# Kernel optimization log

Measured on AMD Instinct MI355X. Metric: run time of the kernel, lower is better.

The kernel has to match this reference:

```python
import jax, jax.numpy as jnp
import numpy as np

D = 768
H = 8
HD = D // H  # 96
DFF = 2048
EPS = 1e-5


def layernorm(x, g, b):
    mu = jnp.mean(x, axis=-1, keepdims=True)
    var = jnp.var(x, axis=-1, keepdims=True)
    return (x - mu) * jax.lax.rsqrt(var + EPS) * g + b


def setup_inputs() -> dict:
    key = jax.random.key(0)
    ks = jax.random.split(key, 12)
    B, L = 4, 1024
    s = lambda fan: 1.0 / np.sqrt(fan)
    return {
        "x": jax.random.normal(ks[0], (B, L, D), jnp.float32),
        "attn_bias": jax.random.normal(ks[1], (B, L, L), jnp.float32),
        "in_proj_w": jax.random.normal(ks[2], (3 * D, D), jnp.float32) * s(D),
        "in_proj_b": jnp.zeros((3 * D,), jnp.float32),
        "out_w": jax.random.normal(ks[3], (D, D), jnp.float32) * s(D),
        "out_b": jnp.zeros((D,), jnp.float32),
        "ff1_w": jax.random.normal(ks[4], (DFF, D), jnp.float32) * s(D),
        "ff1_b": jnp.zeros((DFF,), jnp.float32),
        "ff2_w": jax.random.normal(ks[5], (D, DFF), jnp.float32) * s(DFF),
        "ff2_b": jnp.zeros((D,), jnp.float32),
        "ln1_g": jnp.ones((D,), jnp.float32),
        "ln1_b": jnp.zeros((D,), jnp.float32),
        "ln2_g": jnp.ones((D,), jnp.float32),
        "ln2_b": jnp.zeros((D,), jnp.float32),
    }


def reference(x, attn_bias, in_proj_w, in_proj_b, out_w, out_b,
              ff1_w, ff1_b, ff2_w, ff2_b, ln1_g, ln1_b, ln2_g, ln2_b):
    B, L, _ = x.shape
    # combined QKV projection (torch nn.MultiheadAttention in_proj)
    qkv = x @ in_proj_w.T + in_proj_b  # [B,L,3D]
    q, k, v = jnp.split(qkv, 3, axis=-1)
    q = q.reshape(B, L, H, HD).transpose(0, 2, 1, 3)  # [B,H,L,hd]
    k = k.reshape(B, L, H, HD).transpose(0, 2, 1, 3)
    v = v.reshape(B, L, H, HD).transpose(0, 2, 1, 3)
    scale = 1.0 / np.sqrt(HD)
    scores = jnp.einsum('bhld,bhmd->bhlm', q, k) * scale + attn_bias[:, None, :, :]
    probs = jax.nn.softmax(scores, axis=-1)
    attn = jnp.einsum('bhlm,bhmd->bhld', probs, v)  # [B,H,L,hd]
    attn = attn.transpose(0, 2, 1, 3).reshape(B, L, D)
    attn = attn @ out_w.T + out_b
    x = layernorm(x + attn, ln1_g, ln1_b)
    h = jax.nn.gelu(x @ ff1_w.T + ff1_b, approximate=False) @ ff2_w.T + ff2_b
    x = layernorm(x + h, ln2_g, ln2_b)
    return x
```

## Files before the change

### kernel.cpp

```cpp
#include <hip/hip_runtime.h>

typedef __bf16 bf16x8 __attribute__((ext_vector_type(8)));
typedef float f32x4 __attribute__((ext_vector_type(4)));
typedef unsigned short u16x8 __attribute__((ext_vector_type(8)));
typedef short s16x4 __attribute__((ext_vector_type(4)));

__device__ __forceinline__ unsigned short f2b(float f) {
    union { float f; unsigned u; } v; v.f = f;
    unsigned r = (v.u + 0x7fffu + ((v.u >> 16) & 1u)) >> 16;
    return (unsigned short)r;
}

__device__ __forceinline__ void load_lds16(const void* g, void* l) {
    __builtin_amdgcn_global_load_lds(
        (const __attribute__((address_space(1))) unsigned int*)g,
        (__attribute__((address_space(3))) unsigned int*)l,
        16, 0, 0);
}

__global__ void cvt5_kernel(const float* __restrict__ s0, const float* __restrict__ s1,
                            const float* __restrict__ s2, const float* __restrict__ s3,
                            const float* __restrict__ s4,
                            unsigned short* __restrict__ d0, unsigned short* __restrict__ d1,
                            unsigned short* __restrict__ d2, unsigned short* __restrict__ d3,
                            unsigned short* __restrict__ d4) {
    int i = blockIdx.x * 256 + threadIdx.x;
    const float* s; unsigned short* d; int off;
    if (i < 786432)       { s = s0; d = d0; off = 0; }
    else if (i < 1228800) { s = s1; d = d1; off = 786432; }
    else if (i < 1376256) { s = s2; d = d2; off = 1228800; }
    else if (i < 1769472) { s = s3; d = d3; off = 1376256; }
    else                  { s = s4; d = d4; off = 1769472; }
    i -= off;
    f32x4 v = ((const f32x4*)s)[i];
    s16x4 o;
    o.x = (short)f2b(v.x);
    o.y = (short)f2b(v.y);
    o.z = (short)f2b(v.z);
    o.w = (short)f2b(v.w);
    ((s16x4*)d)[i] = o;
}

template <int EPI>
__global__ __launch_bounds__(256, 5)
void gemm_ho(const unsigned short* __restrict__ A, const unsigned short* __restrict__ Bm,
             const float* __restrict__ bias, void* __restrict__ Cout,
             int M, int N, int K) {
    __shared__ unsigned short As[2][64 * 64];
    __shared__ unsigned short Bs[2][64 * 64];
    const int tid = threadIdx.x, lane = tid & 63, wid = tid >> 6;
    const int l15 = lane & 15, lq = lane >> 4;
    const int wr = wid >> 1, wc = wid & 1;

    const int nwg = gridDim.x * gridDim.y;
    int bid = blockIdx.y * gridDim.x + blockIdx.x;
    bid = (bid & 7) * (nwg >> 3) + (bid >> 3);
    const int bx = bid % gridDim.x, by = bid / gridDim.x;
    const int m0 = by * 64, n0 = bx * 64;

    const int srow = lane >> 3;
    const int scol = ((lane & 7) ^ srow) * 8;
    const int sw = (l15 & 7) << 4;

    f32x4 acc[2][2];
#pragma unroll
    for (int i = 0; i < 2; i++)
#pragma unroll
        for (int j = 0; j < 2; j++) acc[i][j] = 0.0f;

    auto stage = [&](int buf, int kt) {
        const int kb = kt * 64;
#pragma unroll
        for (int i = 0; i < 4; ++i) {
            const int c = wid * 4 + i;
            if (c < 8) {
                load_lds16(A + (size_t)(m0 + c * 8 + srow) * K + kb + scol,
                           (char*)As[buf] + c * 1024);
            } else {
                load_lds16(Bm + (size_t)(n0 + (c - 8) * 8 + srow) * K + kb + scol,
                           (char*)Bs[buf] + (c - 8) * 1024);
            }
        }
    };

    auto compute = [&](int buf) {
#pragma unroll
        for (int kc = 0; kc < 2; ++kc) {
            const int cb = kc * 64;
            bf16x8 af[2], bf[2];
#pragma unroll
            for (int mi = 0; mi < 2; mi++) {
                const int row = wr * 32 + mi * 16 + l15;
                af[mi] = *(const bf16x8*)((const char*)As[buf] + row * 128 + ((cb + lq * 16) ^ sw));
            }
#pragma unroll
            for (int ni = 0; ni < 2; ni++) {
                const int row = wc * 32 + ni * 16 + l15;
                bf[ni] = *(const bf16x8*)((const char*)Bs[buf] + row * 128 + ((cb + lq * 16) ^ sw));
            }
#pragma unroll
            for (int mi = 0; mi < 2; mi++)
#pragma unroll
                for (int ni = 0; ni < 2; ni++)
                    acc[mi][ni] = __builtin_amdgcn_mfma_f32_16x16x32_bf16(af[mi], bf[ni], acc[mi][ni], 0, 0, 0);
        }
    };

    const int nkt = K / 64;
    stage(0, 0);
    stage(1, 1);
    asm volatile("s_waitcnt vmcnt(4)" ::: "memory");
    __builtin_amdgcn_s_barrier();
    int cur = 0;
    for (int t = 0; t < nkt; ++t) {
        compute(cur);
        __builtin_amdgcn_s_barrier();
        if (t + 2 < nkt) {
            stage(cur, t + 2);
            asm volatile("s_waitcnt vmcnt(4)" ::: "memory");
        } else if (t + 1 < nkt) {
            asm volatile("s_waitcnt vmcnt(0)" ::: "memory");
        }
        if (t + 1 < nkt) __builtin_amdgcn_s_barrier();
        cur ^= 1;
    }

#pragma unroll
    for (int mi = 0; mi < 2; mi++) {
#pragma unroll
        for (int ni = 0; ni < 2; ni++) {
            const int col = n0 + wc * 32 + ni * 16 + l15;
            const float bv = bias[col];
#pragma unroll
            for (int r = 0; r < 4; r++) {
                const int row = m0 + wr * 32 + mi * 16 + lq * 4 + r;
                float v = acc[mi][ni][r] + bv;
                if constexpr (EPI == 2) {
                    v = 0.5f * v * (1.0f + erff(v * 0.7071067811865475f));
                }
                if constexpr (EPI == 1) {
                    ((float*)Cout)[(size_t)row * N + col] = v;
                } else {
                    ((unsigned short*)Cout)[(size_t)row * N + col] = f2b(v);
                }
            }
        }
    }
}

__global__ __launch_bounds__(256, 2)
void attn_kernel(const unsigned short* __restrict__ qkv,
                 const float* __restrict__ bias,
                 unsigned short* __restrict__ out) {
    const int L = 1024, TD = 2304, HD = 96;
    const int qt = blockIdx.x, h = blockIdx.y, b = blockIdx.z;
    const int tid = threadIdx.x, lane = tid & 63, wid = tid >> 6;
    const int l15 = lane & 15, lq = lane >> 4;
    const int q0 = qt * 64;
    const float scale = 0.10206207261596576f;

    __shared__ char smem[36352];
    unsigned short (*Ks)[104]    = (unsigned short (*)[104])smem;
    unsigned short (*Vt)[72]     = (unsigned short (*)[72])(smem + 13312);
    unsigned short (*Ps)[16][72] = (unsigned short (*)[16][72])(smem + 27136);
    float (*Ot)[16][100]         = (float (*)[16][100])smem;

    bf16x8 qf[3];
    const int qrow = q0 + wid * 16 + l15;
#pragma unroll
    for (int kc = 0; kc < 3; kc++)
        qf[kc] = *(const bf16x8*)(qkv + (size_t)(b * L + qrow) * TD + h * HD + kc * 32 + lq * 8);

    f32x4 o[6];
#pragma unroll
    for (int df = 0; df < 6; df++) o[df] = 0.0f;
    float lsum[4] = {0.f, 0.f, 0.f, 0.f};

    for (int kv0 = 0; kv0 < L; kv0 += 64) {
#pragma unroll
        for (int i = 0; i < 3; i++) {
            int c = i * 256 + tid;
            int row = c / 12, cc = c % 12;
            *(f32x4*)&Ks[row][cc * 8] =
                *(const f32x4*)(qkv + (size_t)(b * L + kv0 + row) * TD + 768 + h * HD + cc * 8);
        }
#pragma unroll
        for (int i = 0; i < 3; i++) {
            int dblk = i * 4 + wid;
            int m = lane;
            u16x8 v = *(const u16x8*)(qkv + (size_t)(b * L + kv0 + m) * TD + 1536 + h * HD + dblk * 8);
#pragma unroll
            for (int j = 0; j < 8; j++) Vt[dblk * 8 + j][m] = v[j];
        }
        float bpf[4][4];
#pragma unroll
        for (int nf = 0; nf < 4; nf++)
#pragma unroll
            for (int r = 0; r < 4; r++)
                bpf[nf][r] = bias[((size_t)b * L + q0 + wid * 16 + lq * 4 + r) * L
                                  + kv0 + nf * 16 + l15];
        __syncthreads();

        f32x4 s[4];
#pragma unroll
        for (int nf = 0; nf < 4; nf++) s[nf] = 0.0f;
#pragma unroll
        for (int kc = 0; kc < 3; kc++) {
#pragma unroll
            for (int nf = 0; nf < 4; nf++) {
                bf16x8 kf = *(const bf16x8*)&Ks[nf * 16 + l15][kc * 32 + lq * 8];
                s[nf] = __builtin_amdgcn_mfma_f32_16x16x32_bf16(qf[kc], kf, s[nf], 0, 0, 0);
            }
        }
#pragma unroll
        for (int nf = 0; nf < 4; nf++) {
#pragma unroll
            for (int r = 0; r < 4; r++) {
                float p = __expf(s[nf][r] * scale + bpf[nf][r]);
                s[nf][r] = p;
                lsum[r] += p;
            }
        }
#pragma unroll
        for (int nf = 0; nf < 4; nf++)
#pragma unroll
            for (int r = 0; r < 4; r++)
                Ps[wid][lq * 4 + r][nf * 16 + l15] = f2b(s[nf][r]);
        asm volatile("s_waitcnt lgkmcnt(0)" ::: "memory");
#pragma unroll
        for (int kc = 0; kc < 2; kc++) {
            bf16x8 pf = *(const bf16x8*)&Ps[wid][l15][kc * 32 + lq * 8];
#pragma unroll
            for (int df = 0; df < 6; df++) {
                bf16x8 vf = *(const bf16x8*)&Vt[df * 16 + l15][kc * 32 + lq * 8];
                o[df] = __builtin_amdgcn_mfma_f32_16x16x32_bf16(pf, vf, o[df], 0, 0, 0);
            }
        }
        __syncthreads();
    }

#pragma unroll
    for (int r = 0; r < 4; r++) {
#pragma unroll
        for (int d = 1; d < 16; d <<= 1) lsum[r] += __shfl_xor(lsum[r], d, 64);
    }

#pragma unroll
    for (int r = 0; r < 4; r++) {
        float inv = 1.0f / lsum[r];
        const int rl = lq * 4 + r;
#pragma unroll
        for (int df = 0; df < 6; df++) {
            const int cl = df * 16 + l15;
            Ot[wid][rl][cl ^ (lq << 3)] = o[df][r] * inv;
        }
    }
    asm volatile("s_waitcnt lgkmcnt(0)" ::: "memory");
    {
        const int r = lane >> 2, c8 = lane & 3;
        const int rowg = q0 + wid * 16 + r;
#pragma unroll
        for (int it = 0; it < 3; it++) {
            const int oc = c8 + 4 * it;
            const int po = oc ^ ((r >> 2) & 3);
            f32x4 a = *(const f32x4*)&Ot[wid][r][po * 8];
            f32x4 bb = *(const f32x4*)&Ot[wid][r][po * 8 + 4];
            u16x8 p;
#pragma unroll
            for (int e = 0; e < 4; e++) { p[e] = f2b(a[e]); p[e + 4] = f2b(bb[e]); }
            *(u16x8*)&out[((size_t)b * L + rowg) * 768 + h * 96 + oc * 8] = p;
        }
    }
}

template <int WRITE_B>
__global__ __launch_bounds__(256, 4)
void ln_kernel(const float* __restrict__ x, const float* __restrict__ res,
               const float* __restrict__ g, const float* __restrict__ bvec,
               float* __restrict__ outf, unsigned short* __restrict__ outb) {
    const int Dm = 768;
    int row = blockIdx.x;
    int tid = threadIdx.x;
    f32x4 v = {0.f, 0.f, 0.f, 0.f};
    float sum = 0.f, sq = 0.f;
    if (tid < 192) {
        f32x4 xv = ((const f32x4*)(x + (size_t)row * Dm))[tid];
        f32x4 rv = ((const f32x4*)(res + (size_t)row * Dm))[tid];
        v = xv + rv;
        sum = v.x + v.y + v.z + v.w;
        sq = v.x * v.x + v.y * v.y + v.z * v.z + v.w * v.w;
    }
#pragma unroll
    for (int d = 1; d < 64; d <<= 1) {
        sum += __shfl_xor(sum, d, 64);
        sq += __shfl_xor(sq, d, 64);
    }
    __shared__ float ps[8];
    int lane = tid & 63, wid = tid >> 6;
    if (lane == 0) { ps[wid] = sum; ps[wid + 4] = sq; }
    __syncthreads();
    sum = ps[0] + ps[1] + ps[2] + ps[3];
    sq = ps[4] + ps[5] + ps[6] + ps[7];
    float mu = sum * (1.0f / 768.0f);
    float var = sq * (1.0f / 768.0f) - mu * mu;
    float rsg = rsqrtf(var + 1e-5f);
    if (tid < 192) {
        f32x4 gv = ((const f32x4*)g)[tid];
        f32x4 bv = ((const f32x4*)bvec)[tid];
        f32x4 ov;
#pragma unroll
        for (int e = 0; e < 4; e++) ov[e] = (v[e] - mu) * rsg * gv[e] + bv[e];
        ((f32x4*)(outf + (size_t)row * Dm))[tid] = ov;
        if constexpr (WRITE_B) {
            s16x4 pb;
#pragma unroll
            for (int e = 0; e < 4; e++) pb[e] = (short)f2b(ov[e]);
            ((s16x4*)(outb + (size_t)row * Dm))[tid] = pb;
        }
    }
}

extern "C" void kernel_launch(void* const* d_in, const int* in_sizes, int n_in,
                              void* d_out, int out_size, void* d_ws, size_t ws_size,
                              hipStream_t stream) {
    (void)in_sizes; (void)n_in; (void)out_size; (void)ws_size;
    const float* x         = (const float*)d_in[0];
    const float* attn_bias = (const float*)d_in[1];
    const float* in_proj_w = (const float*)d_in[2];
    const float* in_proj_b = (const float*)d_in[3];
    const float* out_w     = (const float*)d_in[4];
    const float* out_b     = (const float*)d_in[5];
    const float* ff1_w     = (const float*)d_in[6];
    const float* ff1_b     = (const float*)d_in[7];
    const float* ff2_w     = (const float*)d_in[8];
    const float* ff2_b     = (const float*)d_in[9];
    const float* ln1_g     = (const float*)d_in[10];
    const float* ln1_b     = (const float*)d_in[11];
    const float* ln2_g     = (const float*)d_in[12];
    const float* ln2_b     = (const float*)d_in[13];

    const int NTOK = 4096;
    char* ws = (char*)d_ws;
    size_t off = 0;
    auto alloc = [&](size_t bytes) { void* p = ws + off; off += (bytes + 255) & ~(size_t)255; return p; };
    unsigned short* xb    = (unsigned short*)alloc((size_t)NTOK * 768 * 2);
    unsigned short* wqkv  = (unsigned short*)alloc((size_t)2304 * 768 * 2);
    unsigned short* wout  = (unsigned short*)alloc((size_t)768 * 768 * 2);
    unsigned short* wff1  = (unsigned short*)alloc((size_t)2048 * 768 * 2);
    unsigned short* wff2  = (unsigned short*)alloc((size_t)768 * 2048 * 2);
    unsigned short* qkvb  = (unsigned short*)alloc((size_t)NTOK * 2304 * 2);
    unsigned short* attnb = (unsigned short*)alloc((size_t)NTOK * 768 * 2);
    float*          aproj = (float*)alloc((size_t)NTOK * 768 * 4);
    float*          x1f   = (float*)alloc((size_t)NTOK * 768 * 4);
    unsigned short* x1b   = (unsigned short*)alloc((size_t)NTOK * 768 * 2);
    unsigned short* h1b  = qkvb;
    float*          ff2o = aproj;

    cvt5_kernel<<<dim3(8448), 256, 0, stream>>>(x, in_proj_w, out_w, ff1_w, ff2_w,
                                                xb, wqkv, wout, wff1, wff2);

    gemm_ho<0><<<dim3(2304 / 64, NTOK / 64), 256, 0, stream>>>(xb, wqkv, in_proj_b, qkvb, NTOK, 2304, 768);
    attn_kernel<<<dim3(16, 8, 4), 256, 0, stream>>>(qkvb, attn_bias, attnb);
    gemm_ho<1><<<dim3(768 / 64, NTOK / 64), 256, 0, stream>>>(attnb, wout, out_b, aproj, NTOK, 768, 768);
    ln_kernel<1><<<dim3(NTOK), 256, 0, stream>>>(x, aproj, ln1_g, ln1_b, x1f, x1b);
    gemm_ho<2><<<dim3(2048 / 64, NTOK / 64), 256, 0, stream>>>(x1b, wff1, ff1_b, h1b, NTOK, 2048, 768);
    gemm_ho<1><<<dim3(768 / 64, NTOK / 64), 256, 0, stream>>>(h1b, wff2, ff2_b, ff2o, NTOK, 768, 2048);
    ln_kernel<0><<<dim3(NTOK), 256, 0, stream>>>(x1f, ff2o, ln2_g, ln2_b, (float*)d_out, nullptr);
}
```

Measured before the change: 171.3 us.

## Precompute exp(bias) in bf16 and software-pipeline K/V/bias loads in attention

A new pre-pass computes exp(attn_bias) once and stores it as bf16, so each of the 8 heads reads a half-size tensor and multiplies it in instead of adding the bias before the exp. The attention loop now issues the next tile's K, V and exp-bias global loads into registers while the current tile computes, then commits them to LDS, with raw s_barrier in place of __syncthreads. This cuts bias bandwidth and hides load latency, at the cost of an extra kernel pass over the bias, more LDS and registers per block, and bf16 rounding of exp(bias). Because the softmax has no max subtraction, a large bias could overflow or lose precision.

Measured after the change: 165.4 us. 1.04x faster.

```diff
diff --git a/kernel.cpp b/kernel.cpp
--- a/kernel.cpp
+++ b/kernel.cpp
@@ -9,6 +9,11 @@
     union { float f; unsigned u; } v; v.f = f;
     unsigned r = (v.u + 0x7fffu + ((v.u >> 16) & 1u)) >> 16;
     return (unsigned short)r;
+}
+
+__device__ __forceinline__ float b2f(unsigned short b) {
+    union { unsigned u; float f; } v; v.u = ((unsigned)b) << 16;
+    return v.f;
 }
 
 __device__ __forceinline__ void load_lds16(const void* g, void* l) {
@@ -41,6 +46,17 @@
     ((s16x4*)d)[i] = o;
 }
 
+__global__ void expb_kernel(const float* __restrict__ bias, unsigned short* __restrict__ eb, int n4) {
+    int i = blockIdx.x * 256 + threadIdx.x;
+    if (i < n4) {
+        f32x4 v = ((const f32x4*)bias)[i];
+        s16x4 o;
+#pragma unroll
+        for (int e = 0; e < 4; e++) o[e] = (short)f2b(__expf(v[e]));
+        ((s16x4*)eb)[i] = o;
+    }
+}
+
 template <int EPI>
 __global__ __launch_bounds__(256, 5)
 void gemm_ho(const unsigned short* __restrict__ A, const unsigned short* __restrict__ Bm,
@@ -150,7 +166,7 @@
 
 __global__ __launch_bounds__(256, 2)
 void attn_kernel(const unsigned short* __restrict__ qkv,
-                 const float* __restrict__ bias,
+                 const unsigned short* __restrict__ eb,
                  unsigned short* __restrict__ out) {
     const int L = 1024, TD = 2304, HD = 96;
     const int qt = blockIdx.x, h = blockIdx.y, b = blockIdx.z;
@@ -159,10 +175,11 @@
     const int q0 = qt * 64;
     const float scale = 0.10206207261596576f;
 
-    __shared__ char smem[36352];
+    __shared__ char smem[45568];
     unsigned short (*Ks)[104]    = (unsigned short (*)[104])smem;
     unsigned short (*Vt)[72]     = (unsigned short (*)[72])(smem + 13312);
     unsigned short (*Ps)[16][72] = (unsigned short (*)[16][72])(smem + 27136);
+    unsigned short (*Ebs)[72]    = (unsigned short (*)[72])(smem + 36352);
     float (*Ot)[16][100]         = (float (*)[16][100])smem;
 
     bf16x8 qf[3];
@@ -171,35 +188,49 @@
     for (int kc = 0; kc < 3; kc++)
         qf[kc] = *(const bf16x8*)(qkv + (size_t)(b * L + qrow) * TD + h * HD + kc * 32 + lq * 8);
 
+    int krow[3], kcc[3];
+#pragma unroll
+    for (int i = 0; i < 3; i++) { int c = i * 256 + tid; krow[i] = c / 12; kcc[i] = c % 12; }
+    int erow[2], ech[2];
+#pragma unroll
+    for (int i = 0; i < 2; i++) { int c = i * 256 + tid; erow[i] = c >> 3; ech[i] = c & 7; }
+
+    f32x4 kreg[3]; u16x8 vreg[3]; u16x8 ereg[2];
+    auto issue = [&](int kv0) {
+#pragma unroll
+        for (int i = 0; i < 3; i++)
+            kreg[i] = *(const f32x4*)(qkv + (size_t)(b * L + kv0 + krow[i]) * TD + 768 + h * HD + kcc[i] * 8);
+#pragma unroll
+        for (int i = 0; i < 3; i++)
+            vreg[i] = *(const u16x8*)(qkv + (size_t)(b * L + kv0 + lane) * TD + 1536 + h * HD + (i * 4 + wid) * 8);
+#pragma unroll
+        for (int i = 0; i < 2; i++)
+            ereg[i] = *(const u16x8*)(eb + (size_t)(b * L + q0 + erow[i]) * L + kv0 + ech[i] * 8);
+    };
+    auto commit = [&]() {
+#pragma unroll
+        for (int i = 0; i < 3; i++) *(f32x4*)&Ks[krow[i]][kcc[i] * 8] = kreg[i];
+#pragma unroll
+        for (int i = 0; i < 3; i++) {
+            const int dblk = i * 4 + wid;
+#pragma unroll
+            for (int j = 0; j < 8; j++) Vt[dblk * 8 + j][lane] = vreg[i][j];
+        }
+#pragma unroll
+        for (int i = 0; i < 2; i++) *(u16x8*)&Ebs[erow[i]][ech[i] * 8] = ereg[i];
+    };
+
     f32x4 o[6];
 #pragma unroll
     for (int df = 0; df < 6; df++) o[df] = 0.0f;
     float lsum[4] = {0.f, 0.f, 0.f, 0.f};
 
-    for (int kv0 = 0; kv0 < L; kv0 += 64) {
-#pragma unroll
-        for (int i = 0; i < 3; i++) {
-            int c = i * 256 + tid;
-            int row = c / 12, cc = c % 12;
-            *(f32x4*)&Ks[row][cc * 8] =
-                *(const f32x4*)(qkv + (size_t)(b * L + kv0 + row) * TD + 768 + h * HD + cc * 8);
-        }
-#pragma unroll
-        for (int i = 0; i < 3; i++) {
-            int dblk = i * 4 + wid;
-            int m = lane;
-            u16x8 v = *(const u16x8*)(qkv + (size_t)(b * L + kv0 + m) * TD + 1536 + h * HD + dblk * 8);
-#pragma unroll
-            for (int j = 0; j < 8; j++) Vt[dblk * 8 + j][m] = v[j];
-        }
-        float bpf[4][4];
-#pragma unroll
-        for (int nf = 0; nf < 4; nf++)
-#pragma unroll
-            for (int r = 0; r < 4; r++)
-                bpf[nf][r] = bias[((size_t)b * L + q0 + wid * 16 + lq * 4 + r) * L
-                                  + kv0 + nf * 16 + l15];
-        __syncthreads();
+    issue(0);
+    for (int t = 0; t < 16; ++t) {
+        asm volatile("s_waitcnt vmcnt(0)" ::: "memory");
+        commit();
+        asm volatile("s_waitcnt lgkmcnt(0)" ::: "memory");
+        __builtin_amdgcn_s_barrier();
 
         f32x4 s[4];
 #pragma unroll
@@ -212,11 +243,14 @@
                 s[nf] = __builtin_amdgcn_mfma_f32_16x16x32_bf16(qf[kc], kf, s[nf], 0, 0, 0);
             }
         }
+        if (t + 1 < 16) issue((t + 1) * 64);
+
 #pragma unroll
         for (int nf = 0; nf < 4; nf++) {
 #pragma unroll
             for (int r = 0; r < 4; r++) {
-                float p = __expf(s[nf][r] * scale + bpf[nf][r]);
+                float ebv = b2f(Ebs[wid * 16 + lq * 4 + r][nf * 16 + l15]);
+                float p = __expf(s[nf][r] * scale) * ebv;
                 s[nf][r] = p;
                 lsum[r] += p;
             }
@@ -236,7 +270,7 @@
                 o[df] = __builtin_amdgcn_mfma_f32_16x16x32_bf16(pf, vf, o[df], 0, 0, 0);
             }
         }
-        __syncthreads();
+        __builtin_amdgcn_s_barrier();
     }
 
 #pragma unroll
@@ -355,12 +389,14 @@
     unsigned short* x1b   = (unsigned short*)alloc((size_t)NTOK * 768 * 2);
     unsigned short* h1b  = qkvb;
     float*          ff2o = aproj;
+    unsigned short* ebuf = (unsigned short*)aproj;
 
     cvt5_kernel<<<dim3(8448), 256, 0, stream>>>(x, in_proj_w, out_w, ff1_w, ff2_w,
                                                 xb, wqkv, wout, wff1, wff2);
+    expb_kernel<<<dim3(4096), 256, 0, stream>>>(attn_bias, ebuf, 1048576);
 
     gemm_ho<0><<<dim3(2304 / 64, NTOK / 64), 256, 0, stream>>>(xb, wqkv, in_proj_b, qkvb, NTOK, 2304, 768);
-    attn_kernel<<<dim3(16, 8, 4), 256, 0, stream>>>(qkvb, attn_bias, attnb);
+    attn_kernel<<<dim3(16, 8, 4), 256, 0, stream>>>(qkvb, ebuf, attnb);
     gemm_ho<1><<<dim3(768 / 64, NTOK / 64), 256, 0, stream>>>(attnb, wout, out_b, aproj, NTOK, 768, 768);
     ln_kernel<1><<<dim3(NTOK), 256, 0, stream>>>(x, aproj, ln1_g, ln1_b, x1f, x1b);
     gemm_ho<2><<<dim3(2048 / 64, NTOK / 64), 256, 0, stream>>>(x1b, wff1, ff1_b, h1b, NTOK, 2048, 768);
```
